# Kernel optimization log

Measured on AMD Instinct MI355X. Metric: run time of the kernel, lower is better.

## Reference

```python
import jax, jax.numpy as jnp
import numpy as np

VOCAB_PRI = 100000
VOCAB_SEC = 100000
EMBED_DIM = 64


def setup_inputs() -> dict:
    key = jax.random.key(0)
    k1, k2, k3, k4 = jax.random.split(key, 4)
    inputs_pri = jax.random.randint(k1, (4096, 200), 0, VOCAB_PRI, dtype=jnp.int64 if jax.config.jax_enable_x64 else jnp.int32)
    inputs_sec = jax.random.randint(k2, (4096, 200), 0, VOCAB_SEC, dtype=jnp.int64 if jax.config.jax_enable_x64 else jnp.int32)
    initrange = 0.01
    emb_pri = jax.random.uniform(k3, (VOCAB_PRI, EMBED_DIM), jnp.float32, -initrange, initrange)
    emb_sec = jax.random.uniform(k4, (VOCAB_SEC, EMBED_DIM), jnp.float32, -initrange, initrange)
    return {"inputs_pri": inputs_pri, "inputs_sec": inputs_sec,
            "emb_pri": emb_pri, "emb_sec": emb_sec}


def _embed_sum(table, idx):
    # gather [B, S, D] then sum over sentence dim -> [B, D]
    # (equivalent to cAdd's per-token accumulation / EmbeddingBag(sum))
    return jnp.sum(table[idx], axis=1)


def reference(inputs_pri, inputs_sec, emb_pri, emb_sec):
    out_pri = _embed_sum(emb_pri, inputs_pri)  # [B, D]
    out_sec = _embed_sum(emb_sec, inputs_sec)  # [B, D]
    return out_pri, out_sec
```

## Files before the change

kernel.cpp:

```cpp
#include <hip/hip_runtime.h>


#define BB 4096
#define SS 200
#define DD 64

__global__ __launch_bounds__(256) void bilingual_embed_sum(
    const int* __restrict__ idx_pri,
    const int* __restrict__ idx_sec,
    const float* __restrict__ emb_pri,
    const float* __restrict__ emb_sec,
    float* __restrict__ out)
{
    __shared__ int sidx[4][SS];

    const int w    = (int)(threadIdx.x >> 6);
    const int lane = (int)(threadIdx.x & 63);
    const int wave = (int)(blockIdx.x * 4 + w);
    const int table = wave >> 12;
    const int b     = wave & (BB - 1);

    const int*   idx = table ? idx_sec : idx_pri;
    const float* emb = table ? emb_sec : emb_pri;
    float* outp = out + (size_t)table * BB * DD + (size_t)b * DD;

    const int* row_idx = idx + b * SS;
    if (lane < SS / 4) {
        const int4 v = ((const int4*)row_idx)[lane];
        sidx[w][lane * 4 + 0] = v.x;
        sidx[w][lane * 4 + 1] = v.y;
        sidx[w][lane * 4 + 2] = v.z;
        sidx[w][lane * 4 + 3] = v.w;
    }
    __syncthreads();

    const int q   = lane >> 4;
    const int l16 = lane & 15;

    float4 acc = make_float4(0.f, 0.f, 0.f, 0.f);

    #pragma unroll 10
    for (int s0 = 0; s0 < SS; s0 += 4) {
        const int i = sidx[w][s0 + q];
        const float4* rp = (const float4*)(emb + (size_t)i * DD);
        const float4 v = rp[l16];
        acc.x += v.x; acc.y += v.y; acc.z += v.z; acc.w += v.w;
    }

    acc.x += __shfl_down(acc.x, 32);
    acc.y += __shfl_down(acc.y, 32);
    acc.z += __shfl_down(acc.z, 32);
    acc.w += __shfl_down(acc.w, 32);
    acc.x += __shfl_down(acc.x, 16);
    acc.y += __shfl_down(acc.y, 16);
    acc.z += __shfl_down(acc.z, 16);
    acc.w += __shfl_down(acc.w, 16);

    if (lane < 16) {
        ((float4*)outp)[l16] = acc;
    }
}

extern "C" void kernel_launch(void* const* d_in, const int* in_sizes, int n_in,
                              void* d_out, int out_size, void* d_ws, size_t ws_size,
                              hipStream_t stream) {
    const int*   idx_pri = (const int*)d_in[0];
    const int*   idx_sec = (const int*)d_in[1];
    const float* emb_pri = (const float*)d_in[2];
    const float* emb_sec = (const float*)d_in[3];
    float* out = (float*)d_out;

    const int n_waves = 2 * BB;
    const int block = 256;
    const int grid = n_waves / (block / 64);

    bilingual_embed_sum<<<grid, block, 0, stream>>>(idx_pri, idx_sec, emb_pri, emb_sec, out);
}
```

Measured before the change: 131.4 us.

## Shard embedding vocab across blocks for cache locality, then combine partial sums

Splits each table's vocabulary into 8 shards and launches one block per (row, shard). Each block filters the row's indices that fall in its shard and sums only those rows into a partial buffer in workspace. A second kernel adds the 8 partials per output. The aim is for concurrent blocks to touch a smaller slice of the table and get better L2/MALL hit rates. The cost is 8x more blocks, each re-reading the 200 indices, shared-memory atomics, a partial-buffer round trip and an extra launch. Because blocks are scheduled roughly in order of block index, the shards are interleaved at any given moment, so the locality gain is doubtful.

After: 158.9 us. 20.9% more time.

```diff
diff --git a/kernel.cpp b/kernel.cpp
--- a/kernel.cpp
+++ b/kernel.cpp
@@ -4,6 +4,94 @@
 #define BB 4096
 #define SS 200
 #define DD 64
+#define NSHARD 8
+#define SHARD_SZ 12500
+#define LISTCAP 216
+
+__global__ __launch_bounds__(256) void embed_shard(
+    const int* __restrict__ idx_pri,
+    const int* __restrict__ idx_sec,
+    const float* __restrict__ emb_pri,
+    const float* __restrict__ emb_sec,
+    float* __restrict__ partial)
+{
+    __shared__ int list[LISTCAP];
+    __shared__ int cnt;
+    __shared__ float4 wred[4][16];
+
+    const int shard = (int)(blockIdx.x & (NSHARD - 1));
+    const int tb    = (int)(blockIdx.x >> 3);
+    const int t     = tb >> 12;
+    const int b     = tb & (BB - 1);
+    const int tid   = (int)threadIdx.x;
+
+    if (tid == 0) cnt = 0;
+    __syncthreads();
+
+    const int*   row_idx = (t ? idx_sec : idx_pri) + b * SS;
+    const float* emb     = t ? emb_sec : emb_pri;
+
+    const int lo = shard * SHARD_SZ;
+    if (tid < SS) {
+        const int i = row_idx[tid];
+        if ((unsigned)(i - lo) < (unsigned)SHARD_SZ) {
+            const int p = atomicAdd(&cnt, 1);
+            list[p] = i;
+        }
+    }
+    __syncthreads();
+    const int n = cnt;
+
+    const int Q   = tid >> 4;
+    const int l16 = tid & 15;
+    float4 acc = make_float4(0.f, 0.f, 0.f, 0.f);
+
+    for (int i0 = 0; i0 < n; i0 += 16) {
+        const int  ii = i0 + Q;
+        const bool ok = ii < n;
+        const int  id = ok ? list[ii] : lo;
+        const float4 v = ((const float4*)(emb + (size_t)id * DD))[l16];
+        if (ok) { acc.x += v.x; acc.y += v.y; acc.z += v.z; acc.w += v.w; }
+    }
+
+    acc.x += __shfl_down(acc.x, 32);
+    acc.y += __shfl_down(acc.y, 32);
+    acc.z += __shfl_down(acc.z, 32);
+    acc.w += __shfl_down(acc.w, 32);
+    acc.x += __shfl_down(acc.x, 16);
+    acc.y += __shfl_down(acc.y, 16);
+    acc.z += __shfl_down(acc.z, 16);
+    acc.w += __shfl_down(acc.w, 16);
+
+    const int w = tid >> 6;
+    if ((tid & 63) < 16) wred[w][l16] = acc;
+    __syncthreads();
+    if (tid < 16) {
+        float4 r = wred[0][tid];
+        const float4 r1 = wred[1][tid];
+        const float4 r2 = wred[2][tid];
+        const float4 r3 = wred[3][tid];
+        r.x += r1.x + r2.x + r3.x;
+        r.y += r1.y + r2.y + r3.y;
+        r.z += r1.z + r2.z + r3.z;
+        r.w += r1.w + r2.w + r3.w;
+        ((float4*)(partial + ((size_t)tb * NSHARD + shard) * DD))[tid] = r;
+    }
+}
+
+__global__ __launch_bounds__(256) void embed_combine(
+    const float* __restrict__ partial,
+    float* __restrict__ out)
+{
+    const int g  = (int)(blockIdx.x * 256 + threadIdx.x);
+    const int tb = g >> 6;
+    const int d  = g & 63;
+    float s = 0.f;
+    #pragma unroll
+    for (int sh = 0; sh < NSHARD; ++sh)
+        s += partial[((size_t)tb * NSHARD + sh) * DD + d];
+    out[g] = s;
+}
 
 __global__ __launch_bounds__(256) void bilingual_embed_sum(
     const int* __restrict__ idx_pri,
@@ -13,7 +101,6 @@
     float* __restrict__ out)
 {
     __shared__ int sidx[4][SS];
-
     const int w    = (int)(threadIdx.x >> 6);
     const int lane = (int)(threadIdx.x & 63);
     const int wave = (int)(blockIdx.x * 4 + w);
@@ -36,14 +123,12 @@
 
     const int q   = lane >> 4;
     const int l16 = lane & 15;
-
     float4 acc = make_float4(0.f, 0.f, 0.f, 0.f);
 
     #pragma unroll 10
     for (int s0 = 0; s0 < SS; s0 += 4) {
         const int i = sidx[w][s0 + q];
-        const float4* rp = (const float4*)(emb + (size_t)i * DD);
-        const float4 v = rp[l16];
+        const float4 v = ((const float4*)(emb + (size_t)i * DD))[l16];
         acc.x += v.x; acc.y += v.y; acc.z += v.z; acc.w += v.w;
     }
 
@@ -56,9 +141,7 @@
     acc.z += __shfl_down(acc.z, 16);
     acc.w += __shfl_down(acc.w, 16);
 
-    if (lane < 16) {
-        ((float4*)outp)[l16] = acc;
-    }
+    if (lane < 16) ((float4*)outp)[l16] = acc;
 }
 
 extern "C" void kernel_launch(void* const* d_in, const int* in_sizes, int n_in,
@@ -70,9 +153,15 @@
     const float* emb_sec = (const float*)d_in[3];
     float* out = (float*)d_out;
 
-    const int n_waves = 2 * BB;
-    const int block = 256;
-    const int grid = n_waves / (block / 64);
+    const size_t ws_need = (size_t)2 * BB * NSHARD * DD * sizeof(float);
 
-    bilingual_embed_sum<<<grid, block, 0, stream>>>(idx_pri, idx_sec, emb_pri, emb_sec, out);
+    if (ws_size >= ws_need) {
+        float* partial = (float*)d_ws;
+        embed_shard<<<2 * BB * NSHARD, 256, 0, stream>>>(
+            idx_pri, idx_sec, emb_pri, emb_sec, partial);
+        embed_combine<<<(2 * BB * DD) / 256, 256, 0, stream>>>(partial, out);
+    } else {
+        bilingual_embed_sum<<<(2 * BB) / 4, 256, 0, stream>>>(
+            idx_pri, idx_sec, emb_pri, emb_sec, out);
+    }
 }
```

## Convert embedding tables to bf16 in workspace before gather-sum

Applied to the files above, without the earlier changes.

Adds a pre-pass kernel that converts each fp32 embedding table to packed bf16 in the workspace. A new gather kernel then reads 128-byte bf16 rows instead of 256-byte fp32 rows and accumulates in fp32. Each block splits a bag across two waves and combines their partial sums through shared memory. The two tables go through the same workspace one after the other, which costs four launches and a full table conversion on every call. Rounding the table values to bf16 adds numerical error against the fp32 reference.

Measured after the change: 123.4 us. 1.07x faster.

```diff
diff --git a/kernel.cpp b/kernel.cpp
--- a/kernel.cpp
+++ b/kernel.cpp
@@ -1,9 +1,88 @@
 #include <hip/hip_runtime.h>
+#include <hip/hip_bf16.h>
 
 
 #define BB 4096
 #define SS 200
 #define DD 64
+#define VOCAB 100000
+
+typedef float vfloat4 __attribute__((ext_vector_type(4)));
+
+__global__ __launch_bounds__(256) void convert_bf16(
+    const float* __restrict__ src,
+    uint2* __restrict__ dst)
+{
+    const size_t g = (size_t)blockIdx.x * 256 + threadIdx.x;
+    const float4 v = ((const float4*)src)[g];
+    const unsigned u0 = __bfloat16_as_ushort(__float2bfloat16(v.x));
+    const unsigned u1 = __bfloat16_as_ushort(__float2bfloat16(v.y));
+    const unsigned u2 = __bfloat16_as_ushort(__float2bfloat16(v.z));
+    const unsigned u3 = __bfloat16_as_ushort(__float2bfloat16(v.w));
+    uint2 o;
+    o.x = u0 | (u1 << 16);
+    o.y = u2 | (u3 << 16);
+    dst[g] = o;
+}
+
+__global__ __launch_bounds__(256) void embed_sum_bf16(
+    const int* __restrict__ idx,
+    const uint2* __restrict__ emb,
+    float* __restrict__ out)
+{
+    __shared__ int sidx[2][SS];
+    __shared__ float4 wred[2][16];
+
+    const int tid  = (int)threadIdx.x;
+    const int w    = tid >> 6;
+    const int lane = tid & 63;
+    const int p    = w >> 1;
+    const int h    = w & 1;
+    const int b    = (int)blockIdx.x * 2 + p;
+
+    const int* ib = idx + (size_t)blockIdx.x * 2 * SS;
+    if (tid < (2 * SS) / 4) {
+        const int4 v = ((const int4*)ib)[tid];
+        int* s = &sidx[0][0];
+        s[tid * 4 + 0] = v.x;
+        s[tid * 4 + 1] = v.y;
+        s[tid * 4 + 2] = v.z;
+        s[tid * 4 + 3] = v.w;
+    }
+    __syncthreads();
+
+    const int q   = lane >> 4;
+    const int l16 = lane & 15;
+
+    float4 acc = make_float4(0.f, 0.f, 0.f, 0.f);
+
+    #pragma unroll 5
+    for (int k = 0; k < 25; ++k) {
+        const int i = sidx[p][8 * k + 4 * h + q];
+        const uint2 v = emb[(size_t)i * 16 + l16];
+        acc.x += __uint_as_float(v.x << 16);
+        acc.y += __uint_as_float(v.x & 0xffff0000u);
+        acc.z += __uint_as_float(v.y << 16);
+        acc.w += __uint_as_float(v.y & 0xffff0000u);
+    }
+
+    acc.x += __shfl_down(acc.x, 32);
+    acc.y += __shfl_down(acc.y, 32);
+    acc.z += __shfl_down(acc.z, 32);
+    acc.w += __shfl_down(acc.w, 32);
+    acc.x += __shfl_down(acc.x, 16);
+    acc.y += __shfl_down(acc.y, 16);
+    acc.z += __shfl_down(acc.z, 16);
+    acc.w += __shfl_down(acc.w, 16);
+
+    if (h == 1 && lane < 16) wred[p][l16] = acc;
+    __syncthreads();
+    if (h == 0 && lane < 16) {
+        const float4 o = wred[p][l16];
+        acc.x += o.x; acc.y += o.y; acc.z += o.z; acc.w += o.w;
+        ((float4*)(out + (size_t)b * DD))[l16] = acc;
+    }
+}
 
 __global__ __launch_bounds__(256) void bilingual_embed_sum(
     const int* __restrict__ idx_pri,
@@ -13,7 +92,6 @@
     float* __restrict__ out)
 {
     __shared__ int sidx[4][SS];
-
     const int w    = (int)(threadIdx.x >> 6);
     const int lane = (int)(threadIdx.x & 63);
     const int wave = (int)(blockIdx.x * 4 + w);
@@ -36,14 +114,12 @@
 
     const int q   = lane >> 4;
     const int l16 = lane & 15;
-
     float4 acc = make_float4(0.f, 0.f, 0.f, 0.f);
 
     #pragma unroll 10
     for (int s0 = 0; s0 < SS; s0 += 4) {
         const int i = sidx[w][s0 + q];
-        const float4* rp = (const float4*)(emb + (size_t)i * DD);
-        const float4 v = rp[l16];
+        const float4 v = ((const float4*)(emb + (size_t)i * DD))[l16];
         acc.x += v.x; acc.y += v.y; acc.z += v.z; acc.w += v.w;
     }
 
@@ -56,9 +132,7 @@
     acc.z += __shfl_down(acc.z, 16);
     acc.w += __shfl_down(acc.w, 16);
 
-    if (lane < 16) {
-        ((float4*)outp)[l16] = acc;
-    }
+    if (lane < 16) ((float4*)outp)[l16] = acc;
 }
 
 extern "C" void kernel_launch(void* const* d_in, const int* in_sizes, int n_in,
@@ -70,9 +144,20 @@
     const float* emb_sec = (const float*)d_in[3];
     float* out = (float*)d_out;
 
-    const int n_waves = 2 * BB;
-    const int block = 256;
-    const int grid = n_waves / (block / 64);
+    const size_t ws_need = (size_t)VOCAB * DD * 2;
 
-    bilingual_embed_sum<<<grid, block, 0, stream>>>(idx_pri, idx_sec, emb_pri, emb_sec, out);
+    if (ws_size >= ws_need) {
+        uint2* tbl = (uint2*)d_ws;
+        const int conv_grid   = (VOCAB * DD / 4) / 256;
+        const int gather_grid = BB / 2;
+
+        convert_bf16<<<conv_grid, 256, 0, stream>>>(emb_pri, tbl);
+        embed_sum_bf16<<<gather_grid, 256, 0, stream>>>(idx_pri, tbl, out);
+        convert_bf16<<<conv_grid, 256, 0, stream>>>(emb_sec, tbl);
+        embed_sum_bf16<<<gather_grid, 256, 0, stream>>>(idx_sec, tbl,
+                                                        out + (size_t)BB * DD);
+    } else {
+        bilingual_embed_sum<<<(2 * BB) / 4, 256, 0, stream>>>(
+            idx_pri, idx_sec, emb_pri, emb_sec, out);
+    }
 }
```
